# Optimization experiments

Measured on AMD Instinct MI355X. Metric: run time of the kernel, lower is better.

Reference implementation:

```python
import jax, jax.numpy as jnp
import numpy as np

N = 100000          # nodes
E = 1600000         # edges
F_IN = 128          # in_channels
C = 32              # hidden_channels (per head)
H = 4               # heads
NEG_SLOPE = 0.2     # PyG GATConv default leaky_relu slope


def setup_inputs() -> dict:
    key = jax.random.key(0)
    ks = jax.random.split(key, 6)
    x = jax.random.normal(ks[0], (N, F_IN), dtype=jnp.float32)
    edge_index = jax.random.randint(ks[1], (2, E), 0, N, dtype=jnp.int32)
    # learned params (PyG GATConv: lin weight, att_src, att_dst, bias)
    W = jax.random.normal(ks[2], (F_IN, H * C), dtype=jnp.float32) * (1.0 / np.sqrt(F_IN))
    att_src = jax.random.normal(ks[3], (H, C), dtype=jnp.float32) * 0.1
    att_dst = jax.random.normal(ks[4], (H, C), dtype=jnp.float32) * 0.1
    bias = jnp.zeros((H * C,), dtype=jnp.float32)
    return {"x": x, "edge_index": edge_index, "W": W,
            "att_src": att_src, "att_dst": att_dst, "bias": bias}


def reference(x, edge_index, W, att_src, att_dst, bias):
    # linear projection, split into heads: [N, H, C]
    h = (x @ W).reshape(N, H, C)
    # per-node attention terms: [N, H]
    a_src = jnp.einsum('nhc,hc->nh', h, att_src)
    a_dst = jnp.einsum('nhc,hc->nh', h, att_dst)
    src, dst = edge_index[0], edge_index[1]
    # edge-wise logits: [E, H]
    alpha = jax.nn.leaky_relu(a_src[src] + a_dst[dst], NEG_SLOPE)
    # segment softmax over incoming edges of each dst node
    amax = jax.ops.segment_max(alpha, dst, num_segments=N)       # [N, H]
    amax = jnp.where(jnp.isfinite(amax), amax, 0.0)
    ex = jnp.exp(alpha - amax[dst])                              # [E, H]
    denom = jax.ops.segment_sum(ex, dst, num_segments=N)         # [N, H]
    alpha = ex / (denom[dst] + 1e-16)                            # [E, H]
    # weighted messages, scatter-add to dst: [N, H, C]
    msg = h[src] * alpha[:, :, None]
    out = jax.ops.segment_sum(msg, dst, num_segments=N)
    out = out.reshape(N, H * C) + bias
    return jax.nn.elu(out)
```

## Files before the change

kernel.cpp:

```cpp
#include <hip/hip_runtime.h>
#include <hip/hip_bf16.h>
#include <math.h>

#define N_NODES 100000
#define N_EDGES 1600000
#define NEG_SLOPE 0.2f

#define NB_BUCKET 782
#define ST_CAP 2560

#define OFF_H     0
#define OFF_ASRC  25600000
#define OFF_ADST  27200000
#define OFF_NODE  28800000
#define OFF_BCUR  29600000
#define OFF_TMP   29604096
#define OFF_WHT   37611776
#define OFF_WLT   37644544
#define OFF_WAH   37677312
#define OFF_WAL   37681408

typedef __attribute__((ext_vector_type(8))) __bf16 bf16x8;
typedef __attribute__((ext_vector_type(4))) float  f32x4;
union BF8 { unsigned u32[4]; bf16x8 v; };

__device__ __forceinline__ float leaky(float x) {
    return fmaxf(x, NEG_SLOPE * x);
}
__device__ __forceinline__ float sel4(int h, float a, float b, float c, float d) {
    return h == 0 ? a : (h == 1 ? b : (h == 2 ? c : d));
}
__device__ __forceinline__ float2 bf2_to_f2(unsigned int u) {
    float2 r;
    r.x = __uint_as_float(u << 16);
    r.y = __uint_as_float(u & 0xffff0000u);
    return r;
}
__device__ __forceinline__ unsigned bf16_rne(float f) {
    const unsigned b = __float_as_uint(f);
    return ((b + 0x7FFFu + ((b >> 16) & 1u)) >> 16) & 0xFFFFu;
}
__device__ __forceinline__ float bf16_tof(unsigned hb) {
    return __uint_as_float(hb << 16);
}
__device__ __forceinline__ void wave_lds_fence() {
    asm volatile("s_waitcnt lgkmcnt(0)" ::: "memory");
    __builtin_amdgcn_sched_barrier(0);
}

__global__ __launch_bounds__(256) void wprep_kernel(
    const float* __restrict__ W, const float* __restrict__ att_src,
    const float* __restrict__ att_dst,
    ushort* __restrict__ WhT, ushort* __restrict__ WlT,
    ushort* __restrict__ WAh, ushort* __restrict__ WAl,
    int* __restrict__ bcur)
{
    const int idx = blockIdx.x * 256 + threadIdx.x;
    const int n = idx >> 7, k = idx & 127;
    const float w  = W[k * 128 + n];
    const unsigned hb = bf16_rne(w);
    const float rs = w - bf16_tof(hb);
    WhT[n * 128 + k] = (ushort)hb;
    WlT[n * 128 + k] = (ushort)bf16_rne(rs);

    if (idx < 2048) {
        const int j = idx >> 7;
        float v = 0.f;
        if (j < 8) {
            const int hh = j & 3;
            const float* att = (j < 4) ? att_src : att_dst;
#pragma unroll
            for (int c = 0; c < 32; ++c)
                v = fmaf(W[k * 128 + hh * 32 + c], att[hh * 32 + c], v);
        }
        const unsigned ab = bf16_rne(v);
        WAh[j * 128 + k] = (ushort)ab;
        WAl[j * 128 + k] = (ushort)bf16_rne(v - bf16_tof(ab));
    }
    if (idx < NB_BUCKET) bcur[idx] = 0;
}

__global__ __launch_bounds__(256, 2) void gemm_mfma_kernel(
    const float* __restrict__ x, const ushort* __restrict__ WhT,
    const ushort* __restrict__ WlT, const ushort* __restrict__ WAh,
    const ushort* __restrict__ WAl,
    ushort* __restrict__ h_u16, float* __restrict__ a_src, float* __restrict__ a_dst)
{
    const int wv   = threadIdx.x >> 6;
    const int lane = threadIdx.x & 63;
    const int c15  = lane & 15;
    const int kg   = lane >> 4;
    const int r0g  = blockIdx.x * 128 + wv * 32;

    bf16x8 ah[2][4], al[2][4];
#pragma unroll
    for (int mt = 0; mt < 2; ++mt) {
        int row = r0g + mt * 16 + c15;
        row = row < N_NODES ? row : N_NODES - 1;
        const float4* xp = (const float4*)&x[(size_t)row * 128];
#pragma unroll
        for (int ks = 0; ks < 4; ++ks) {
            const int kb = ks * 32 + kg * 8;
            const float4 fa = xp[kb >> 2];
            const float4 fb = xp[(kb >> 2) + 1];
            const float f[8] = {fa.x, fa.y, fa.z, fa.w, fb.x, fb.y, fb.z, fb.w};
            BF8 H, L;
#pragma unroll
            for (int j = 0; j < 4; ++j) {
                const unsigned h0 = bf16_rne(f[2 * j + 0]);
                const unsigned h1 = bf16_rne(f[2 * j + 1]);
                const unsigned l0 = bf16_rne(f[2 * j + 0] - bf16_tof(h0));
                const unsigned l1 = bf16_rne(f[2 * j + 1] - bf16_tof(h1));
                H.u32[j] = h0 | (h1 << 16);
                L.u32[j] = l0 | (l1 << 16);
            }
            ah[mt][ks] = H.v;
            al[mt][ks] = L.v;
        }
    }

    f32x4 acc[2][8];
    f32x4 acca[2];
#pragma unroll
    for (int mt = 0; mt < 2; ++mt) {
        acca[mt] = (f32x4){0.f, 0.f, 0.f, 0.f};
#pragma unroll
        for (int nt = 0; nt < 8; ++nt)
            acc[mt][nt] = (f32x4){0.f, 0.f, 0.f, 0.f};
    }

#pragma unroll
    for (int ks = 0; ks < 4; ++ks) {
        const int kb = ks * 32 + kg * 8;
#pragma unroll
        for (int nt = 0; nt < 8; ++nt) {
            const int col = nt * 16 + c15;
            const bf16x8 bh = *(const bf16x8*)&WhT[col * 128 + kb];
            const bf16x8 bl = *(const bf16x8*)&WlT[col * 128 + kb];
            acc[0][nt] = __builtin_amdgcn_mfma_f32_16x16x32_bf16(ah[0][ks], bh, acc[0][nt], 0, 0, 0);
            acc[1][nt] = __builtin_amdgcn_mfma_f32_16x16x32_bf16(ah[1][ks], bh, acc[1][nt], 0, 0, 0);
            acc[0][nt] = __builtin_amdgcn_mfma_f32_16x16x32_bf16(al[0][ks], bh, acc[0][nt], 0, 0, 0);
            acc[1][nt] = __builtin_amdgcn_mfma_f32_16x16x32_bf16(al[1][ks], bh, acc[1][nt], 0, 0, 0);
            acc[0][nt] = __builtin_amdgcn_mfma_f32_16x16x32_bf16(ah[0][ks], bl, acc[0][nt], 0, 0, 0);
            acc[1][nt] = __builtin_amdgcn_mfma_f32_16x16x32_bf16(ah[1][ks], bl, acc[1][nt], 0, 0, 0);
        }
        const bf16x8 bha = *(const bf16x8*)&WAh[c15 * 128 + kb];
        const bf16x8 bla = *(const bf16x8*)&WAl[c15 * 128 + kb];
        acca[0] = __builtin_amdgcn_mfma_f32_16x16x32_bf16(ah[0][ks], bha, acca[0], 0, 0, 0);
        acca[1] = __builtin_amdgcn_mfma_f32_16x16x32_bf16(ah[1][ks], bha, acca[1], 0, 0, 0);
        acca[0] = __builtin_amdgcn_mfma_f32_16x16x32_bf16(al[0][ks], bha, acca[0], 0, 0, 0);
        acca[1] = __builtin_amdgcn_mfma_f32_16x16x32_bf16(al[1][ks], bha, acca[1], 0, 0, 0);
        acca[0] = __builtin_amdgcn_mfma_f32_16x16x32_bf16(ah[0][ks], bla, acca[0], 0, 0, 0);
        acca[1] = __builtin_amdgcn_mfma_f32_16x16x32_bf16(ah[1][ks], bla, acca[1], 0, 0, 0);
    }

#pragma unroll
    for (int mt = 0; mt < 2; ++mt) {
#pragma unroll
        for (int reg = 0; reg < 4; ++reg) {
            const int row = r0g + mt * 16 + kg * 4 + reg;
            if (row >= N_NODES) continue;
#pragma unroll
            for (int nt = 0; nt < 8; ++nt)
                h_u16[(size_t)row * 128 + nt * 16 + c15] =
                    (ushort)bf16_rne(acc[mt][nt][reg]);
            if (c15 < 4)
                a_src[row * 4 + c15] = acca[mt][reg];
            else if (c15 < 8)
                a_dst[row * 4 + (c15 - 4)] = acca[mt][reg];
        }
    }
}

#define S1_EPB 6250
__global__ __launch_bounds__(256) void scat_kernel(
    const int* __restrict__ src, const int* __restrict__ dst,
    int* __restrict__ bcur, unsigned int* __restrict__ tmp)
{
    __shared__ int cnt[NB_BUCKET];
    __shared__ int dstash[S1_EPB];
    const int tid = threadIdx.x;
    for (int i = tid; i < NB_BUCKET; i += 256) cnt[i] = 0;
    __syncthreads();
    const int e0 = blockIdx.x * S1_EPB;
    for (int i = tid; i < S1_EPB; i += 256) {
        const int d = dst[e0 + i];
        dstash[i] = d;
        atomicAdd(&cnt[d >> 7], 1);
    }
    __syncthreads();
    for (int b = tid; b < NB_BUCKET; b += 256) {
        const int c = cnt[b];
        cnt[b] = c ? (b * ST_CAP + atomicAdd(&bcur[b], c)) : 0;
    }
    __syncthreads();
    for (int i = tid; i < S1_EPB; i += 256) {
        const int d = dstash[i];
        const int s = src[e0 + i];
        const int p = atomicAdd(&cnt[d >> 7], 1);
        tmp[p] = ((unsigned int)s << 7) | (unsigned int)(d & 127);
    }
}

__global__ __launch_bounds__(256) void phaseB_kernel(
    const unsigned int* __restrict__ tmp, const int* __restrict__ bcur,
    int2* __restrict__ node_info, int* __restrict__ csr)
{
    __shared__ unsigned int st[ST_CAP];
    __shared__ int hist[128];
    __shared__ int cur[128];
    __shared__ int wtot[4];

    const int b    = blockIdx.x;
    const int tid  = threadIdx.x;
    const int lane = tid & 63;
    const int wv   = tid >> 6;
    const int base = b * ST_CAP;
    int cnt = bcur[b];
    cnt = cnt < ST_CAP ? cnt : ST_CAP;

    if (tid < 128) hist[tid] = 0;
    __syncthreads();

    for (int i = tid; i < cnt; i += 256) {
        const unsigned int v = tmp[base + i];
        st[i] = v;
        atomicAdd(&hist[v & 127], 1);
    }
    __syncthreads();

    const int hv = (tid < 128) ? hist[tid] : 0;
    int sv = hv;
#pragma unroll
    for (int off = 1; off < 64; off <<= 1) {
        int u = __shfl_up(sv, off);
        if (lane >= off) sv += u;
    }
    if (lane == 63) wtot[wv] = sv;
    __syncthreads();
    const int wpre = (wv > 0 ? wtot[0] : 0) + (wv > 1 ? wtot[1] : 0) + (wv > 2 ? wtot[2] : 0);
    if (tid < 128) {
        const int excl = wpre + sv - hv;
        cur[tid] = excl;
        const int node = (b << 7) + tid;
        if (node < N_NODES) node_info[node] = make_int2(base + excl, hv);
    }
    __syncthreads();

    for (int i = tid; i < cnt; i += 256) {
        const unsigned int v = st[i];
        const int p = atomicAdd(&cur[v & 127], 1);
        csr[base + p] = (int)(v >> 7);
    }
}

__global__ __launch_bounds__(256, 4) void gat_agg_kernel(
    const int* __restrict__ csr_src, const int2* __restrict__ node_info,
    const __hip_bfloat162* __restrict__ h_bf,
    const float* __restrict__ a_src, const float* __restrict__ a_dst,
    const float* __restrict__ bias, float* __restrict__ out)
{
    __shared__ float4 stage[4][128];

    const int wv   = threadIdx.x >> 6;
    const int lane = threadIdx.x & 63;
    const int node = blockIdx.x * 4 + wv;

    const int2 nf  = node_info[node];
    const int start = nf.x;
    const int deg   = nf.y;

    const float4 ad4 = ((const float4*)a_dst)[node];

    float sf = __int_as_float(0);
    float e0 = 0.f, e1 = 0.f, e2 = 0.f, e3 = 0.f;
    if (lane < deg) {
        const int s = csr_src[start + lane];
        sf = __int_as_float(s);
        const float4 as4 = ((const float4*)a_src)[s];
        e0 = __expf(leaky(as4.x + ad4.x));
        e1 = __expf(leaky(as4.y + ad4.y));
        e2 = __expf(leaky(as4.z + ad4.z));
        e3 = __expf(leaky(as4.w + ad4.w));
    }
    stage[wv][lane * 2 + 0] = make_float4(sf, e0, sf, e1);
    stage[wv][lane * 2 + 1] = make_float4(sf, e2, sf, e3);
    wave_lds_fence();

    if (deg <= 64) {
        const int qw   = lane >> 4;
        const int cpos = lane & 15;
        const int hsub = cpos >> 2;
        const float2* sp = (const float2*)&stage[wv][0];
        const uint4*  hp = (const uint4*)h_bf;

        float acc[8];
#pragma unroll
        for (int i = 0; i < 8; ++i) acc[i] = 0.f;
        float den = 0.f;

        for (int j = 0; j < deg; j += 16) {
#pragma unroll
            for (int u = 0; u < 4; ++u) {
                const float2 se = sp[(j + u * 4 + qw) * 4 + hsub];
                const float ev = se.y;
                const unsigned s = (unsigned)__float_as_int(se.x);
                const uint4 hv = hp[(size_t)(s * 16u + (unsigned)cpos)];
                float2 f;
                f = bf2_to_f2(hv.x);
                acc[0] = fmaf(ev, f.x, acc[0]);
                acc[1] = fmaf(ev, f.y, acc[1]);
                f = bf2_to_f2(hv.y);
                acc[2] = fmaf(ev, f.x, acc[2]);
                acc[3] = fmaf(ev, f.y, acc[3]);
                f = bf2_to_f2(hv.z);
                acc[4] = fmaf(ev, f.x, acc[4]);
                acc[5] = fmaf(ev, f.y, acc[5]);
                f = bf2_to_f2(hv.w);
                acc[6] = fmaf(ev, f.x, acc[6]);
                acc[7] = fmaf(ev, f.y, acc[7]);
                den += ev;
            }
        }

#pragma unroll
        for (int i = 0; i < 8; ++i) acc[i] += __shfl_xor(acc[i], 16);
#pragma unroll
        for (int i = 0; i < 8; ++i) acc[i] += __shfl_xor(acc[i], 32);
        den += __shfl_xor(den, 16);
        den += __shfl_xor(den, 32);

        const float inv = 1.0f / (den + 1e-16f);
#pragma unroll
        for (int i = 0; i < 8; ++i) acc[i] *= inv;

        if (qw == 0) {
            float4* sf4 = (float4*)&stage[wv][0];
            sf4[cpos * 2 + 0] = make_float4(acc[0], acc[1], acc[2], acc[3]);
            sf4[cpos * 2 + 1] = make_float4(acc[4], acc[5], acc[6], acc[7]);
        }
        wave_lds_fence();
        const float2 v  = ((const float2*)&stage[wv][0])[lane];
        const float2 b2 = ((const float2*)bias)[lane];
        float ox = v.x + b2.x;
        float oy = v.y + b2.y;
        ox = ox > 0.f ? ox : __expf(ox) - 1.f;
        oy = oy > 0.f ? oy : __expf(oy) - 1.f;
        ((float2*)out)[(size_t)node * 64 + lane] = make_float2(ox, oy);
    } else {
        const int hidx = lane >> 4;
        const float adh = sel4(hidx, ad4.x, ad4.y, ad4.z, ad4.w);
        float2 acc = {0.f, 0.f};
        float  den = 0.f;
        for (int j = 0; j < deg; ++j) {
            const int s = csr_src[start + j];
            const float ash = a_src[s * 4 + hidx];
            const float ex = __expf(leaky(ash + adh));
            const float2 f = __bfloat1622float2(h_bf[(size_t)s * 64 + lane]);
            acc.x += ex * f.x;
            acc.y += ex * f.y;
            den   += ex;
        }
        const float inv = 1.0f / (den + 1e-16f);
        const float2 b2 = ((const float2*)bias)[lane];
        float ox = acc.x * inv + b2.x;
        float oy = acc.y * inv + b2.y;
        ox = ox > 0.f ? ox : expm1f(ox);
        oy = oy > 0.f ? oy : expm1f(oy);
        ((float2*)out)[(size_t)node * 64 + lane] = make_float2(ox, oy);
    }
}

extern "C" void kernel_launch(void* const* d_in, const int* in_sizes, int n_in,
                              void* d_out, int out_size, void* d_ws, size_t ws_size,
                              hipStream_t stream)
{
    const float* x       = (const float*)d_in[0];
    const int*   ei      = (const int*)  d_in[1];
    const float* W       = (const float*)d_in[2];
    const float* att_src = (const float*)d_in[3];
    const float* att_dst = (const float*)d_in[4];
    const float* bias    = (const float*)d_in[5];
    float*       out     = (float*)d_out;

    char* ws = (char*)d_ws;
    ushort* h_u16 = (ushort*)(ws + OFF_H);
    __hip_bfloat162* h_bf = (__hip_bfloat162*)(ws + OFF_H);
    float* a_src = (float*)(ws + OFF_ASRC);
    float* a_dst = (float*)(ws + OFF_ADST);
    int2*  ninfo = (int2*) (ws + OFF_NODE);
    int*   bcur  = (int*)  (ws + OFF_BCUR);
    unsigned int* tmp = (unsigned int*)(ws + OFF_TMP);
    int*   csr   = (int*)  (ws + OFF_TMP);
    ushort* WhT  = (ushort*)(ws + OFF_WHT);
    ushort* WlT  = (ushort*)(ws + OFF_WLT);
    ushort* WAh  = (ushort*)(ws + OFF_WAH);
    ushort* WAl  = (ushort*)(ws + OFF_WAL);

    const int* srcp = ei;
    const int* dstp = ei + N_EDGES;

    wprep_kernel<<<64, 256, 0, stream>>>(W, att_src, att_dst, WhT, WlT, WAh, WAl, bcur);

    gemm_mfma_kernel<<<(N_NODES + 127) / 128, 256, 0, stream>>>(
        x, WhT, WlT, WAh, WAl, h_u16, a_src, a_dst);

    scat_kernel<<<N_EDGES / S1_EPB, 256, 0, stream>>>(srcp, dstp, bcur, tmp);
    phaseB_kernel<<<NB_BUCKET, 256, 0, stream>>>(tmp, bcur, ninfo, csr);

    gat_agg_kernel<<<N_NODES / 4, 256, 0, stream>>>(
        csr, ninfo, h_bf, a_src, a_dst, bias, out);
}
```

Baseline: 268.8 us.

## Merge GEMM and edge-scatter kernels into one launch with block specialization

```diff
diff --git a/kernel.cpp b/kernel.cpp
--- a/kernel.cpp
+++ b/kernel.cpp
@@ -80,17 +80,53 @@
     if (idx < NB_BUCKET) bcur[idx] = 0;
 }
 
-__global__ __launch_bounds__(256, 2) void gemm_mfma_kernel(
+#define S1_EPB 6250
+#define FAT_SCAT_BLOCKS 256
+#define FAT_GEMM_BLOCKS 782
+
+__global__ __launch_bounds__(256, 2) void fat_kernel(
     const float* __restrict__ x, const ushort* __restrict__ WhT,
     const ushort* __restrict__ WlT, const ushort* __restrict__ WAh,
     const ushort* __restrict__ WAl,
-    ushort* __restrict__ h_u16, float* __restrict__ a_src, float* __restrict__ a_dst)
+    ushort* __restrict__ h_u16, float* __restrict__ a_src, float* __restrict__ a_dst,
+    const int* __restrict__ src, const int* __restrict__ dst,
+    int* __restrict__ bcur, unsigned int* __restrict__ tmp)
 {
-    const int wv   = threadIdx.x >> 6;
-    const int lane = threadIdx.x & 63;
+    __shared__ int s_cnt[NB_BUCKET];
+    __shared__ int s_dstash[S1_EPB];
+
+    const int tid = threadIdx.x;
+
+    if (blockIdx.x < FAT_SCAT_BLOCKS) {
+        for (int i = tid; i < NB_BUCKET; i += 256) s_cnt[i] = 0;
+        __syncthreads();
+        const int e0 = blockIdx.x * S1_EPB;
+        for (int i = tid; i < S1_EPB; i += 256) {
+            const int d = dst[e0 + i];
+            s_dstash[i] = d;
+            atomicAdd(&s_cnt[d >> 7], 1);
+        }
+        __syncthreads();
+        for (int b = tid; b < NB_BUCKET; b += 256) {
+            const int c = s_cnt[b];
+            s_cnt[b] = c ? (b * ST_CAP + atomicAdd(&bcur[b], c)) : 0;
+        }
+        __syncthreads();
+        for (int i = tid; i < S1_EPB; i += 256) {
+            const int d = s_dstash[i];
+            const int s = src[e0 + i];
+            const int p = atomicAdd(&s_cnt[d >> 7], 1);
+            tmp[p] = ((unsigned int)s << 7) | (unsigned int)(d & 127);
+        }
+        return;
+    }
+
+    const int gb   = blockIdx.x - FAT_SCAT_BLOCKS;
+    const int wv   = tid >> 6;
+    const int lane = tid & 63;
     const int c15  = lane & 15;
     const int kg   = lane >> 4;
-    const int r0g  = blockIdx.x * 128 + wv * 32;
+    const int r0g  = gb * 128 + wv * 32;
 
     bf16x8 ah[2][4], al[2][4];
 #pragma unroll
@@ -169,36 +205,6 @@
             else if (c15 < 8)
                 a_dst[row * 4 + (c15 - 4)] = acca[mt][reg];
         }
-    }
-}
-
-#define S1_EPB 6250
-__global__ __launch_bounds__(256) void scat_kernel(
-    const int* __restrict__ src, const int* __restrict__ dst,
-    int* __restrict__ bcur, unsigned int* __restrict__ tmp)
-{
-    __shared__ int cnt[NB_BUCKET];
-    __shared__ int dstash[S1_EPB];
-    const int tid = threadIdx.x;
-    for (int i = tid; i < NB_BUCKET; i += 256) cnt[i] = 0;
-    __syncthreads();
-    const int e0 = blockIdx.x * S1_EPB;
-    for (int i = tid; i < S1_EPB; i += 256) {
-        const int d = dst[e0 + i];
-        dstash[i] = d;
-        atomicAdd(&cnt[d >> 7], 1);
-    }
-    __syncthreads();
-    for (int b = tid; b < NB_BUCKET; b += 256) {
-        const int c = cnt[b];
-        cnt[b] = c ? (b * ST_CAP + atomicAdd(&bcur[b], c)) : 0;
-    }
-    __syncthreads();
-    for (int i = tid; i < S1_EPB; i += 256) {
-        const int d = dstash[i];
-        const int s = src[e0 + i];
-        const int p = atomicAdd(&cnt[d >> 7], 1);
-        tmp[p] = ((unsigned int)s << 7) | (unsigned int)(d & 127);
     }
 }
 
@@ -402,10 +408,10 @@
 
     wprep_kernel<<<64, 256, 0, stream>>>(W, att_src, att_dst, WhT, WlT, WAh, WAl, bcur);
 
-    gemm_mfma_kernel<<<(N_NODES + 127) / 128, 256, 0, stream>>>(
-        x, WhT, WlT, WAh, WAl, h_u16, a_src, a_dst);
-
-    scat_kernel<<<N_EDGES / S1_EPB, 256, 0, stream>>>(srcp, dstp, bcur, tmp);
+    fat_kernel<<<FAT_SCAT_BLOCKS + FAT_GEMM_BLOCKS, 256, 0, stream>>>(
+        x, WhT, WlT, WAh, WAl, h_u16, a_src, a_dst,
+        srcp, dstp, bcur, tmp);
+
     phaseB_kernel<<<NB_BUCKET, 256, 0, stream>>>(tmp, bcur, ninfo, csr);
 
     gat_agg_kernel<<<N_NODES / 4, 256, 0, stream>>>(
```

New measurement: 253.8 us. -5.6%, faster.
